# Optimization experiments

Hardware: AMD Instinct MI355X
Metric: run time of the kernel (lower is better)

The kernel has to match this reference:

```python
import jax, jax.numpy as jnp
import numpy as np

# ---- module hyperparameters (from init_kwargs / tracker defaults) ----
D_MODEL = 512
D_HEAD = 512
LAMBDA_0 = 1.0        # A_0 = I / lambda_0
FIXED_LAMBDA = 1.0    # fixed penalty magnitude -> U = sqrt(lambda) * K (then / sqrt(d_head))
STAB_EPS = 1e-6       # InversePenaltyTracker.stabilization_eps
PERIODIC_EPS = 1e-6   # InversePenaltyTracker.periodic_eps
PERIOD = 128          # InversePenaltyTracker.period (periodic re-regularization)
EXPLODE_EPS = 1e-5    # fallback_add_explode coefficient
NORM_THRESH = 1000.0  # explosion detection threshold on Frobenius norms


def setup_inputs() -> dict:
    key = jax.random.key(0)
    ks = jax.random.split(key, 9)
    B, T, d = 8, 2048, D_MODEL
    s = 1.0 / np.sqrt(d)
    f32 = jnp.float32
    return {
        "x": jax.random.normal(ks[0], (B, T, d), f32),
        "Wq": (jax.random.normal(ks[1], (D_HEAD, d), f32) * s),
        "bq": jax.random.normal(ks[2], (D_HEAD,), f32) * 0.02,
        "Wk": (jax.random.normal(ks[3], (D_HEAD, d), f32) * s),
        "bk": jax.random.normal(ks[4], (D_HEAD,), f32) * 0.02,
        "Wv": (jax.random.normal(ks[5], (D_HEAD, d), f32) * s),
        "bv": jax.random.normal(ks[6], (D_HEAD,), f32) * 0.02,
        "Wo": (jax.random.normal(ks[7], (d, D_HEAD), f32) * s),
        "bo": jax.random.normal(ks[8], (d,), f32) * 0.02,
    }


def _vla_forward(x, Wq, bq, Wk, bk, Wv, bv, Wo, bo):
    B, T, _ = x.shape
    d = D_HEAD
    # projections (nn.Linear: x @ W.T + b)
    Q = jnp.einsum('btd,hd->bth', x, Wq) + bq
    K = jnp.einsum('btd,hd->bth', x, Wk) + bk
    V = jnp.einsum('btd,hd->bth', x, Wv) + bv

    # PenaltyBuilder (rank 1, fixed lambda): u_t = sqrt(lambda) * k_t, then / sqrt(d_head)
    U = (jnp.sqrt(jnp.float32(FIXED_LAMBDA)) / jnp.sqrt(jnp.float32(d))) * K
    s_seq = jnp.sum(K * Q, axis=-1)                                   # (B,T)
    Vn = V / (jnp.linalg.norm(V, axis=-1, keepdims=True) + 1e-6)      # (B,T,d)

    I = jnp.eye(d, dtype=jnp.float32)
    A0 = jnp.zeros((B, d, d), jnp.float32) + I / LAMBDA_0
    S0 = jnp.zeros((B, d, d), jnp.float32)

    def step(carry, inp):
        A, S = carry
        q, u, s_t, vn, t = inp  # q,u,vn: (B,d); s_t: (B,); t: scalar int
        # Sherman-Morrison rank-1 inverse update with stabilization
        z = jnp.einsum('bij,bj->bi', A, u)
        dot = jnp.sum(u * z, axis=-1)
        delta = jnp.maximum(1.0 + dot, 1e-6)
        unstable = (jnp.abs(delta) < STAB_EPS) | ~jnp.isfinite(delta)
        safe = jnp.where(unstable, 1.0, delta)
        upd = (z[:, :, None] * z[:, None, :]) / safe[:, None, None]
        A = jnp.where(unstable[:, None, None], A + STAB_EPS * I, A - upd)
        # periodic re-regularization (inv_step = t+1)
        A = jnp.where(((t + 1) % PERIOD) == 0, A + PERIODIC_EPS * I, A)
        # alpha_t = s_t * (A u_t)
        z2 = jnp.einsum('bij,bj->bi', A, u)
        alpha = s_t[:, None] * z2
        # memory update S += v_norm alpha^T
        S = S + vn[:, :, None] * alpha[:, None, :]
        # explosion guard
        Sn = jnp.linalg.norm(S.reshape(S.shape[0], -1), axis=-1)
        An = jnp.linalg.norm(A.reshape(A.shape[0], -1), axis=-1)
        A = jnp.where(((Sn > NORM_THRESH) | (An > NORM_THRESH))[:, None, None],
                      A + EXPLODE_EPS * I, A)
        o = jnp.einsum('bij,bj->bi', S, q)
        return (A, S), o

    xs = (jnp.swapaxes(Q, 0, 1), jnp.swapaxes(U, 0, 1),
          jnp.swapaxes(s_seq, 0, 1), jnp.swapaxes(Vn, 0, 1),
          jnp.arange(T))
    _, O = jax.lax.scan(step, (A0, S0), xs)    # O: (T,B,d)
    O = jnp.swapaxes(O, 0, 1)                  # (B,T,d)
    return jnp.einsum('bth,dh->btd', O, Wo) + bo


def reference(x, Wq, bq, Wk, bk, Wv, bv, Wo, bo):
    return _vla_forward(x, Wq, bq, Wk, bk, Wv, bv, Wo, bo)
```

## Files before the change

### kernel.cpp

```cpp
#include <hip/hip_runtime.h>
#include <hip/hip_bf16.h>

#define BB 8
#define TT 2048
#define DD 512
#define LL 128
#define NC 16
#define ETH 512

typedef unsigned short u16;
typedef unsigned int u32;
typedef __attribute__((ext_vector_type(8))) short bf16x8v;
typedef __attribute__((ext_vector_type(4))) float f32x4v;

__device__ __forceinline__ float bf2f(u32 h) { return __uint_as_float(h << 16); }
__device__ __forceinline__ u16 f2bf(float f) {
    u32 u = __float_as_uint(f);
    u += 0x7fffu + ((u >> 16) & 1u);
    return (u16)(u >> 16);
}
__device__ __forceinline__ float wred64(float v) {
    #pragma unroll
    for (int off = 32; off; off >>= 1) v += __shfl_xor(v, off);
    return v;
// ... 253 lines not shown
            acc[i][j] = (f32x4v){0.f, 0.f, 0.f, 0.f};

    const u16* gA[4]; const u16* gB[4];
    #pragma unroll
    for (int i = 0; i < 4; ++i) {
        const int idx = i * 256 + tid, row = idx >> 3, c = idx & 7;
        const int kb = c ^ (row & 7);
        gA[i] = Ab + (size_t)row * 512 + kb * 8;
        gB[i] = Bb + (size_t)row * 512 + kb * 8;
    }
    for (int k0 = 0; k0 < 512; k0 += 64) {
        __syncthreads();
        #pragma unroll
        for (int i = 0; i < 4; ++i) {
            const int dst = (i * 256 + wave * 64) * 8;
            __builtin_amdgcn_global_load_lds(
                (__attribute__((address_space(1))) void*)(gA[i] + k0),
                (__attribute__((address_space(3))) void*)(Agh + dst), 16, 0, 0);
            __builtin_amdgcn_global_load_lds(
                (__attribute__((address_space(1))) void*)(gB[i] + k0),
                (__attribute__((address_space(3))) void*)(Bgh + dst), 16, 0, 0);
        }
        asm volatile("s_waitcnt vmcnt(0)" ::: "memory");
        __syncthreads();

        const int l15 = lane & 15, lhi = lane >> 4;
        bf16x8v af[4][2], bfr[4][2];
        #pragma unroll
        for (int mf = 0; mf < 4; ++mf) {
            const int row = wm * 64 + mf * 16 + l15, sw = (row & 7) << 4;
            #pragma unroll
            for (int ks = 0; ks < 2; ++ks) {
                const int kb2 = (ks * 64 + lhi * 16) ^ sw;
                af[mf][ks] = *(const bf16x8v*)((const char*)Agh + row * 128 + kb2);
            }
        }
        #pragma unroll
        for (int nf = 0; nf < 4; ++nf) {
            const int row = wn * 64 + nf * 16 + l15, sw = (row & 7) << 4;
            #pragma unroll
            for (int ks = 0; ks < 2; ++ks) {
                const int kb2 = (ks * 64 + lhi * 16) ^ sw;
                bfr[nf][ks] = *(const bf16x8v*)((const char*)Bgh + row * 128 + kb2);
            }
        }
        #pragma unroll
        for (int ks = 0; ks < 2; ++ks)
            #pragma unroll
            for (int mf = 0; mf < 4; ++mf)
                #pragma unroll
                for (int nf = 0; nf < 4; ++nf)
                    acc[mf][nf] = __builtin_amdgcn_mfma_f32_16x16x32_bf16(
                        af[mf][ks], bfr[nf][ks], acc[mf][nf], 0, 0, 0);
    }
    const int l15 = lane & 15, lhi = lane >> 4;
    #pragma unroll
    for (int mf = 0; mf < 4; ++mf)
        #pragma unroll
        for (int nf = 0; nf < 4; ++nf) {
            const int n = wn * 64 + nf * 16 + l15;
            #pragma unroll
            for (int r = 0; r < 4; ++r) {
                const int m = wm * 64 + mf * 16 + lhi * 4 + r;
                Cq[(size_t)m * 128 + n] = acc[mf][nf][r];
            }
        }
}

__global__ __launch_bounds__(256)
void mfk1_kernel(const u16* __restrict__ Abf, const u16* __restrict__ Ut,
                 float* __restrict__ Wm)
{
    __shared__ u16 Ah[128 * 64];
    __shared__ u16 Bh[128 * 64];
    const int tid = threadIdx.x, wave = tid >> 6, lane = tid & 63;
    const int wm = wave >> 1, wn = wave & 1;
    const int m0 = blockIdx.x * 128;
    const int bz = blockIdx.z;

    f32x4v acc[4][4];
    #pragma unroll
    for (int i = 0; i < 4; ++i)
        #pragma unroll
        for (int j = 0; j < 4; ++j)
            acc[i][j] = (f32x4v){0.f, 0.f, 0.f, 0.f};

    const u16* Abase = Abf + (size_t)bz * 262144;
    const u16* Bbase = Ut + (size_t)bz * 1048576;
    const u16* gA[4]; const u16* gB[4];
    #pragma unroll
    for (int i = 0; i < 4; ++i) {
        const int idx = i * 256 + tid, row = idx >> 3, c = idx & 7;
        const int kb = c ^ (row & 7);
        gA[i] = Abase + (size_t)(m0 + row) * 512 + kb * 8;
        gB[i] = Bbase + (size_t)row * 512 + kb * 8;
    }
    for (int k0 = 0; k0 < 512; k0 += 64) {
        __syncthreads();
        #pragma unroll
        for (int i = 0; i < 4; ++i) {
            const int dst = (i * 256 + wave * 64) * 8;
            __builtin_amdgcn_global_load_lds(
                (__attribute__((address_space(1))) void*)(gA[i] + k0),
                (__attribute__((address_space(3))) void*)(Ah + dst), 16, 0, 0);
            __builtin_amdgcn_global_load_lds(
                (__attribute__((address_space(1))) void*)(gB[i] + k0),
                (__attribute__((address_space(3))) void*)(Bh + dst), 16, 0, 0);
        }
        asm volatile("s_waitcnt vmcnt(0)" ::: "memory");
        __syncthreads();

        const int l15 = lane & 15, lhi = lane >> 4;
        bf16x8v af[4][2], bfr[4][2];
        #pragma unroll
        for (int mf = 0; mf < 4; ++mf) {
            const int row = wm * 64 + mf * 16 + l15, sw = (row & 7) << 4;
            #pragma unroll
            for (int ks = 0; ks < 2; ++ks) {
                const int kb2 = (ks * 64 + lhi * 16) ^ sw;
                af[mf][ks] = *(const bf16x8v*)((const char*)Ah + row * 128 + kb2);
            }
        }
        #pragma unroll
        for (int nf = 0; nf < 4; ++nf) {
            const int row = wn * 64 + nf * 16 + l15, sw = (row & 7) << 4;
            #pragma unroll
            for (int ks = 0; ks < 2; ++ks) {
                const int kb2 = (ks * 64 + lhi * 16) ^ sw;
                bfr[nf][ks] = *(const bf16x8v*)((const char*)Bh + row * 128 + kb2);
            }
        }
        #pragma unroll
        for (int ks = 0; ks < 2; ++ks)
            #pragma unroll
            for (int mf = 0; mf < 4; ++mf)
                #pragma unroll
                for (int nf = 0; nf < 4; ++nf)
                    acc[mf][nf] = __builtin_amdgcn_mfma_f32_16x16x32_bf16(
                        af[mf][ks], bfr[nf][ks], acc[mf][nf], 0, 0, 0);
    }
    const int l15 = lane & 15, lhi = lane >> 4;
    float* C = Wm + (size_t)bz * 65536;
    #pragma unroll
    for (int mf = 0; mf < 4; ++mf)
        #pragma unroll
        for (int nf = 0; nf < 4; ++nf) {
            const int n = wn * 64 + nf * 16 + l15;
            #pragma unroll
            for (int r = 0; r < 4; ++r) {
                const int m = m0 + wm * 64 + mf * 16 + lhi * 4 + r;
                C[(size_t)m * 128 + n] = acc[mf][nf][r];
            }
        }
}

__global__ __launch_bounds__(256)
void prep_kernel(const u16* __restrict__ Qb, const u16* __restrict__ Ub,
                 u16* __restrict__ Vb, float* __restrict__ sseq)
{
    const int lane = threadIdx.x & 63, wid = threadIdx.x >> 6;
    const int row = blockIdx.x * 4 + wid;
    const size_t base = (size_t)row * DD;
    const uint4 qr = *(const uint4*)(Qb + base + lane * 8);
    const uint4 ur = *(const uint4*)(Ub + base + lane * 8);
    const uint4 vr = *(const uint4*)(Vb + base + lane * 8);
    float q[8], u[8], v[8];
    unpack8(qr, q); unpack8(ur, u); unpack8(vr, v);
    float sd = 0.f, nv = 0.f;
    #pragma unroll
    for (int e = 0; e < 8; ++e) { sd = fmaf(q[e], u[e], sd); nv = fmaf(v[e], v[e], nv); }
    #pragma unroll
    for (int off = 32; off; off >>= 1) { sd += __shfl_xor(sd, off); nv += __shfl_xor(nv, off); }
    if (lane == 0) sseq[row] = sd * 22.627416997969522f;
    const float inv = 1.f / (sqrtf(nv) + 1e-6f);
    uint4 o;
    o.x = (u32)f2bf(v[0] * inv) | ((u32)f2bf(v[1] * inv) << 16);
    o.y = (u32)f2bf(v[2] * inv) | ((u32)f2bf(v[3] * inv) << 16);
    o.z = (u32)f2bf(v[4] * inv) | ((u32)f2bf(v[5] * inv) << 16);
    o.w = (u32)f2bf(v[6] * inv) | ((u32)f2bf(v[7] * inv) << 16);
    *(uint4*)(Vb + base + lane * 8) = o;
}

__global__ __launch_bounds__(256)
void init_kernel(float4* __restrict__ A4, float4* __restrict__ S4,
                 ushort4* __restrict__ Sbf4, ushort4* __restrict__ Abf4,
                 float* __restrict__ SnSq, float* __restrict__ AnAcc)
{
    const int gtid = blockIdx.x * 256 + threadIdx.x;
    const int N4 = BB * DD * DD / 4;
    const ushort4 z4 = {0, 0, 0, 0};
    for (int idx = gtid; idx < N4; idx += gridDim.x * 256) {
        const int e0 = idx << 2;
        const int r = (e0 >> 9) & 511;
        const int c = e0 & 511;
        float4 v;
        v.x = (c + 0 == r) ? 1.f : 0.f;
        v.y = (c + 1 == r) ? 1.f : 0.f;
        v.z = (c + 2 == r) ? 1.f : 0.f;
        v.w = (c + 3 == r) ? 1.f : 0.f;
        A4[idx] = v;
        S4[idx] = make_float4(0.f, 0.f, 0.f, 0.f);
        Sbf4[idx] = z4;
        if (Abf4) {
            ushort4 a;
            a.x = (c + 0 == r) ? 0x3F80 : 0;
            a.y = (c + 1 == r) ? 0x3F80 : 0;
            a.z = (c + 2 == r) ? 0x3F80 : 0;
            a.w = (c + 3 == r) ? 0x3F80 : 0;
            Abf4[idx] = a;
        }
    }
    if (gtid < BB) { SnSq[gtid] = 0.f; AnAcc[gtid] = 512.f; }
}

struct GP {
    int alay, blay, epi;
    const void* Ap; const void* Bp;
    void* Cp; float* Cio;
    const float* gdiag; float* anacc;
    const float* invdp; const float* cap; const float* cbp;
    const u16* Ulastp; float* Zsp; float* Alphap;
    u16* albt; u16* sbf; u16* abf;
    int lda, ldb, ldc, K;
    long sA, sB, sC, sCio;
};

__device__ __forceinline__ void gemm_body(const GP& p, const int bz) {
    __shared__ __align__(16) float As[32][68];
    __shared__ __align__(16) float Bs[32][68];
    const int m0 = blockIdx.x * 64, n0 = blockIdx.y * 64;
    const int tid = threadIdx.x, tx = tid & 15, ty = tid >> 4;
    float acc[4][4] = {};
    for (int k0 = 0; k0 < p.K; k0 += 32) {
        if (p.alay == 0) {
            const float* A = (const float*)p.Ap + (size_t)bz * p.sA;
            #pragma unroll
            for (int h = 0; h < 2; ++h) {
                const int g = tid + h * 256, m = g >> 3, k4 = (g & 7) * 4;
                const float4 r = *(const float4*)(A + (size_t)(m0 + m) * p.lda + k0 + k4);
                As[k4][m] = r.x; As[k4+1][m] = r.y; As[k4+2][m] = r.z; As[k4+3][m] = r.w;
            }
        } else if (p.alay == 2) {
            const u16* A = (const u16*)p.Ap + (size_t)bz * p.sA;
            #pragma unroll
            for (int h = 0; h < 2; ++h) {
                const int g = tid + h * 256, m = g >> 3, k4 = (g & 7) * 4;
                const ushort4 r = *(const ushort4*)(A + (size_t)(m0 + m) * p.lda + k0 + k4);
                As[k4][m]=bf2f(r.x); As[k4+1][m]=bf2f(r.y); As[k4+2][m]=bf2f(r.z); As[k4+3][m]=bf2f(r.w);
            }
        } else if (p.alay == 1 || p.alay == 4) {
            const float* A = (const float*)p.Ap + (size_t)bz * p.sA;
            #pragma unroll
            for (int h = 0; h < 2; ++h) {
                const int g = tid + h * 256, k = g >> 4, m4 = (g & 15) * 4;
                float4 r = *(const float4*)(A + (size_t)(k0 + k) * p.lda + m0 + m4);
                if (p.alay == 4) {
                    const int kg = k0 + k, mg = m0 + m4;
                    if (kg > mg + 0) r.x = 0.f;
                    if (kg > mg + 1) r.y = 0.f;
                    if (kg > mg + 2) r.z = 0.f;
                    if (kg > mg + 3) r.w = 0.f;
                }
                As[k][m4] = r.x; As[k][m4+1] = r.y; As[k][m4+2] = r.z; As[k][m4+3] = r.w;
            }
        } else {
            const u16* A = (const u16*)p.Ap + (size_t)bz * p.sA;
            #pragma unroll
            for (int h = 0; h < 2; ++h) {
                const int g = tid + h * 256, k = g >> 4, m4 = (g & 15) * 4;
                const ushort4 r = *(const ushort4*)(A + (size_t)(k0 + k) * p.lda + m0 + m4);
                As[k][m4]=bf2f(r.x); As[k][m4+1]=bf2f(r.y); As[k][m4+2]=bf2f(r.z); As[k][m4+3]=bf2f(r.w);
            }
        }
        if (p.blay == 0) {
            const float* B = (const float*)p.Bp + (size_t)bz * p.sB;
            #pragma unroll
            for (int h = 0; h < 2; ++h) {
                const int g = tid + h * 256, k = g >> 4, n4 = (g & 15) * 4;
                const float4 r = *(const float4*)(B + (size_t)(k0 + k) * p.ldb + n0 + n4);
                Bs[k][n4] = r.x; Bs[k][n4+1] = r.y; Bs[k][n4+2] = r.z; Bs[k][n4+3] = r.w;
            }
        } else if (p.blay == 2) {
            const u16* B = (const u16*)p.Bp + (size_t)bz * p.sB;
            #pragma unroll
            for (int h = 0; h < 2; ++h) {
                const int g = tid + h * 256, k = g >> 4, n4 = (g & 15) * 4;
                const ushort4 r = *(const ushort4*)(B + (size_t)(k0 + k) * p.ldb + n0 + n4);
                Bs[k][n4]=bf2f(r.x); Bs[k][n4+1]=bf2f(r.y); Bs[k][n4+2]=bf2f(r.z); Bs[k][n4+3]=bf2f(r.w);
            }
        } else if (p.blay == 1) {
            const float* B = (const float*)p.Bp + (size_t)bz * p.sB;
            #pragma unroll
            for (int h = 0; h < 2; ++h) {
                const int g = tid + h * 256, n = g >> 3, k4 = (g & 7) * 4;
                const float4 r = *(const float4*)(B + (size_t)(n0 + n) * p.ldb + k0 + k4);
                Bs[k4][n] = r.x; Bs[k4+1][n] = r.y; Bs[k4+2][n] = r.z; Bs[k4+3][n] = r.w;
            }
        } else {
            const u16* B = (const u16*)p.Bp + (size_t)bz * p.sB;
            #pragma unroll
            for (int h = 0; h < 2; ++h) {
                const int g = tid + h * 256, n = g >> 3, k4 = (g & 7) * 4;
                const ushort4 r = *(const ushort4*)(B + (size_t)(n0 + n) * p.ldb + k0 + k4);
                Bs[k4][n]=bf2f(r.x); Bs[k4+1][n]=bf2f(r.y); Bs[k4+2][n]=bf2f(r.z); Bs[k4+3][n]=bf2f(r.w);
            }
        }
        __syncthreads();
        #pragma unroll
        for (int kk = 0; kk < 32; ++kk) {
            const float4 xa = *(const float4*)&As[kk][ty * 4];
            const float4 wb = *(const float4*)&Bs[kk][tx * 4];
            const float xv[4] = {xa.x, xa.y, xa.z, xa.w};
            const float wv[4] = {wb.x, wb.y, wb.z, wb.w};
            #pragma unroll
            for (int i = 0; i < 4; ++i)
                #pragma unroll
                for (int j = 0; j < 4; ++j)
                    acc[i][j] = fmaf(xv[i], wv[j], acc[i][j]);
        }
        __syncthreads();
    }
    const int mb = m0 + ty * 4, nb = n0 + tx * 4;
    if (p.epi == 0) {
        float* C = (float*)p.Cp + (size_t)bz * p.sC;
        #pragma unroll
        for (int i = 0; i < 4; ++i)
            #pragma unroll
            for (int j = 0; j < 4; ++j)
                C[(size_t)(mb + i) * p.ldc + nb + j] = acc[i][j];
    } else if (p.epi == 1) {
        float* C = p.Cio + (size_t)bz * p.sCio;
        const float gd = p.gdiag[bz];
        float v2 = 0.f;
        #pragma unroll
        for (int i = 0; i < 4; ++i)
            #pragma unroll
            for (int j = 0; j < 4; ++j) {
                const size_t idx = (size_t)(mb + i) * p.ldc + nb + j;
                float v = C[idx] - acc[i][j] + ((mb + i) == (nb + j) ? gd : 0.f);
                C[idx] = v;
                if (p.abf) p.abf[(size_t)bz * p.sCio + idx] = f2bf(v);
                v2 = fmaf(v, v, v2);
            }
        v2 = wred64(v2);
        if ((tid & 63) == 0) atomicAdd(p.anacc + bz, v2);
    } else if (p.epi == 2) {
        float* C = p.Cio + (size_t)bz * p.sCio;
        u16* SB = p.sbf + (size_t)bz * p.sCio;
        #pragma unroll
        for (int i = 0; i < 4; ++i)
            #pragma unroll
            for (int j = 0; j < 4; ++j) {
                const size_t idx = (size_t)(mb + i) * p.ldc + nb + j;
                const float v = C[idx] + acc[i][j];
                C[idx] = v;
                SB[idx] = f2bf(v);
            }
    } else if (p.epi == 3) {
        u16* O = (u16*)p.Cp + (size_t)bz * p.sC;
        const float* OB = p.Cio + (size_t)bz * p.sCio;
        #pragma unroll
        for (int i = 0; i < 4; ++i)
            #pragma unroll
            for (int j = 0; j < 4; ++j)
                O[(size_t)(mb + i) * p.ldc + nb + j] =
                    f2bf(acc[i][j] + OB[(size_t)(nb + j) * 256 + mb + i]);
    } else {
        float* Zb  = (float*)p.Cp + (size_t)bz * 65536;
        float* Zsb = p.Zsp + (size_t)bz * 65536;
        float* Apb = p.Alphap + (size_t)bz * 65536;
        #pragma unroll
        for (int j = 0; j < 4; ++j) {
            const int n = nb + j;
            const float iv = p.invdp[bz * 128 + n];
            const float cav = p.cap[bz * 128 + n];
            const float cbv = p.cbp[bz * 128 + n];
            #pragma unroll
            for (int i = 0; i < 4; ++i) {
                const int m = mb + i;
                const float z = acc[i][j];
                const size_t o = (size_t)m * 128 + n;
                Zb[o] = z;
                Zsb[o] = z * iv;
                float a = z * cav;
                if (cbv != 0.f) a = fmaf(cbv, bf2f(p.Ulastp[(size_t)bz * 1048576 + m]), a);
                Apb[o] = a;
                p.albt[(size_t)bz * 65536 + (size_t)n * 512 + m] = f2bf(a);
            }
        }
    }
}

__global__ __launch_bounds__(256) void gemmx(GP p) { gemm_body(p, blockIdx.z); }

__global__ __launch_bounds__(256)
void lvl5_kernel(const u16* Sb, const u16* AlT, const float* Alpha,
                 const u16* Qt, const u16* Vnt,
                 float* P, float* Ga, float* Gv, float* OBSA, float* dsum)
{
    const int z = blockIdx.z;
    if (z < 8) {
        mfk6_body(Sb, Qt, AlT, Vnt, OBSA, dsum, z);
        return;
    }
    if (blockIdx.x != 0 || blockIdx.y != 0) return;
    const int zz = z - 8, b = zz / 3, j = zz - b * 3;
    const u16* Ab = (j == 2) ? (Vnt + (size_t)b * 1048576) : (AlT + (size_t)b * 65536);
    const u16* Bb = (j == 0) ? (Qt + (size_t)b * 1048576)
                  : (j == 1) ? (AlT + (size_t)b * 65536)
                             : (Vnt + (size_t)b * 1048576);
    float* Cq = ((j == 0) ? P : (j == 1) ? Ga : Gv) + (size_t)b * 16384;
    mfg_body(Ab, Bb, Cq);
}

__global__ __launch_bounds__(256)
void lvl7_kernel(const float* P, const u16* Vnt, u16* Obt, const float* OBSA,
                 const float* Alpha, const float* Zs, const float* Z,
                 float* S, u16* Sbf, float* A, u16* Abf,
                 const float* gdiag, float* AnAcc)
{
    const int z = blockIdx.z;
    GP p{};
    if (z < 8) {
        p.alay = 0; p.Ap = Zs; p.lda = 128; p.sA = 65536;
        p.blay = 1; p.Bp = Z; p.ldb = 128; p.sB = 65536;
        p.epi = 1; p.Cio = A; p.sCio = 262144; p.ldc = 512;
        p.gdiag = gdiag; p.anacc = AnAcc; p.abf = Abf; p.K = 128;
        gemm_body(p, z);
    } else if (z < 16) {
        p.alay = 3; p.Ap = Vnt; p.lda = 512; p.sA = 1048576;
        p.blay = 1; p.Bp = Alpha; p.ldb = 128; p.sB = 65536;
        p.epi = 2; p.Cio = S; p.sbf = Sbf; p.sCio = 262144; p.ldc = 512; p.K = 128;
        gemm_body(p, z - 8);
    } else {
        if (blockIdx.x >= 2) return;
        p.alay = 4; p.Ap = P; p.lda = 128; p.sA = 16384;
        p.blay = 2; p.Bp = Vnt; p.ldb = 512; p.sB = 1048576;
        p.epi = 3; p.Cp = Obt; p.ldc = 512; p.sC = 1048576;
        p.Cio = (float*)OBSA; p.sCio = 131072; p.K = 128;
        gemm_body(p, z - 16);
    }
}

__global__ __launch_bounds__(512)
void elim_kernel(const float* __restrict__ G, float* __restrict__ Tg,
                 const float* __restrict__ sseq, float* __restrict__ invd,
                 float* __restrict__ ca, float* __restrict__ cb,
                 float* __restrict__ dsum_g, const int t0)
{
    const int b = blockIdx.x, tid = threadIdx.x, lane = tid & 63, wave = tid >> 6;
    __shared__ __align__(16) float E[128][132];
    __shared__ __align__(16) float Cs[128][132];
    __shared__ __align__(16) float Scr[2368];
    __shared__ float del[128];
    float (*Tm)[132] = E;
    float (*LpT)[132] = (float(*)[132])Scr;
    float (*SpT)[132] = (float(*)[132])(Scr + 1056);

    {
        const float4* Gb = (const float4*)(G + (size_t)b * 16384);
        for (int idx = tid; idx < 4096; idx += ETH) {
            const int r = idx >> 5, c4 = idx & 31;
            ((float4*)&E[r][0])[c4] = Gb[idx];
        }
    }
    if (tid < 128) dsum_g[b * 128 + tid] = 0.f;
    __syncthreads();

    for (int p = 0; p < 16; ++p) {
        const int pc0 = p * 8;
        if (wave == 0) {
            float pr0[8], pr1[8];
            #pragma unroll
            for (int j = 0; j < 8; ++j) {
                pr0[j] = E[pc0 + j][lane];
                pr1[j] = E[pc0 + j][64 + lane];
            }
            float dl[8];
            const bool hi = (pc0 >= 64);
            #pragma unroll
            for (int j = 0; j < 8; ++j) {
                const int t = pc0 + j;
                const int pl = t & 63;
                float prow[8];
                #pragma unroll
                for (int c = 0; c < 8; ++c) {
                    const float v0 = __shfl(pr0[c], pl);
                    const float v1 = __shfl(pr1[c], pl);
                    prow[c] = hi ? v1 : v0;
                }
                const float d = fmaxf(1.f + prow[j], 1e-6f);
                dl[j] = d;
                const float inv = 1.f / d;
                if (lane > t) {
                    const float coef = pr0[j] * inv;
                    #pragma unroll
                    for (int c = j + 1; c < 8; ++c) pr0[c] = fmaf(-coef, prow[c], pr0[c]);
                }
                if (lane + 64 > t) {
                    const float coef = pr1[j] * inv;
                    #pragma unroll
                    for (int c = j + 1; c < 8; ++c) pr1[c] = fmaf(-coef, prow[c], pr1[c]);
                }
            }
            #pragma unroll
            for (int j = 0; j < 8; ++j) {
                const float idj = 1.f / dl[j];
                const int t = pc0 + j;
                {
                    const bool below = (lane > t);
                    const float y = below ? pr0[j] : 0.f;
                    const float l = y * idj;
                    LpT[j][lane] = l; SpT[j][lane] = y; Cs[t][lane] = l;
                }
                {
                    const int r = lane + 64;
                    const bool below = (r > t);
                    const float y = below ? pr1[j] : 0.f;
                    const float l = y * idj;
                    LpT[j][r] = l; SpT[j][r] = y; Cs[t][r] = l;
                }
            }
            if (lane < 8) del[pc0 + lane] = dl[lane];
        }
        __syncthreads();
        const int r0b = pc0 + 8;
        if (r0b < 128) {
            const int nrows = 128 - r0b;
            const int c40 = r0b >> 2, nc4 = 32 - c40;
            for (int idx = tid; idx < nrows * nc4; idx += ETH) {
                const int rr = idx / nc4, cc = idx - rr * nc4;
                const int r = r0b + rr, c4 = c40 + cc;
                float4 e = ((float4*)&E[r][0])[c4];
                #pragma unroll
                for (int j = 0; j < 8; ++j) {
                    const float lv = LpT[j][r];
                    const float4 sv = ((const float4*)&SpT[j][0])[c4];
                    e.x = fmaf(-lv, sv.x, e.x);
                    e.y = fmaf(-lv, sv.y, e.y);
                    e.z = fmaf(-lv, sv.z, e.z);
                    e.w = fmaf(-lv, sv.w, e.w);
                }
                ((float4*)&E[r][0])[c4] = e;
            }
        }
        __syncthreads();
    }

    for (int idx = tid; idx < 4224; idx += ETH)
        ((float4*)&Tm[0][0])[idx] = make_float4(0.f, 0.f, 0.f, 0.f);
    __syncthreads();
    if (tid < 128) Tm[tid][tid] = 1.f;
    __syncthreads();
    {
        const int g = tid >> 3, c = tid & 7;
        if (g < 16) {
            for (int r2 = c - 1; r2 >= 0; --r2) {
                float s = 0.f;
                for (int kk = r2 + 1; kk <= c; ++kk)
                    s = fmaf(Cs[8 * g + r2][8 * g + kk],
                             (kk == c) ? 1.f : Tm[8 * g + kk][8 * g + c], s);
                Tm[8 * g + r2][8 * g + c] = -s;
            }
        }
    }
    __syncthreads();
    for (int s = 8; s <= 64; s <<= 1) {
        const int npairs = 64 / s;
        const int nj = (s == 64) ? 32 : s;
        const int stride = nj + 4;
        const int nj4 = nj >> 2;
        const int Nel = npairs * s * nj4;
        const int nhalf = (s == 64) ? 2 : 1;
        for (int jh = 0; jh < nhalf; ++jh) {
            for (int idx = tid; idx < Nel; idx += ETH) {
                const int p2 = idx / (s * nj4), rem = idx - p2 * s * nj4;
                const int i = rem / nj4, j4 = rem - i * nj4;
                const int I0 = 2 * s * p2, J0 = I0 + s;
                const int jc = j4 * 4 + jh * 32;
                float4 x = make_float4(0.f, 0.f, 0.f, 0.f);
                for (int k = 0; k < s; ++k) {
                    const float cv = Cs[I0 + i][J0 + k];
                    const float4 tv = *(const float4*)&Tm[J0 + k][J0 + jc];
                    x.x = fmaf(cv, tv.x, x.x);
                    x.y = fmaf(cv, tv.y, x.y);
                    x.z = fmaf(cv, tv.z, x.z);
                    x.w = fmaf(cv, tv.w, x.w);
                }
                *(float4*)&Scr[p2 * s * stride + i * stride + j4 * 4] = x;
            }
            __syncthreads();
            for (int idx = tid; idx < Nel; idx += ETH) {
                const int p2 = idx / (s * nj4), rem = idx - p2 * s * nj4;
                const int i = rem / nj4, j4 = rem - i * nj4;
                const int I0 = 2 * s * p2, J0 = I0 + s;
                const int jc = j4 * 4 + jh * 32;
                float4 y = make_float4(0.f, 0.f, 0.f, 0.f);
                for (int k = 0; k < s; ++k) {
                    const float tv = Tm[I0 + i][I0 + k];
                    const float4 xv = *(const float4*)&Scr[p2 * s * stride + k * stride + j4 * 4];
                    y.x = fmaf(tv, xv.x, y.x);
                    y.y = fmaf(tv, xv.y, y.y);
                    y.z = fmaf(tv, xv.z, y.z);
                    y.w = fmaf(tv, xv.w, y.w);
                }
                float4 o;
                o.x = -y.x; o.y = -y.y; o.z = -y.z; o.w = -y.w;
                *(float4*)&Tm[I0 + i][J0 + jc] = o;
            }
            __syncthreads();
        }
    }
    {
        float4* Tgb = (float4*)(Tg + (size_t)b * 16384);
        for (int idx = tid; idx < 4096; idx += ETH) {
            const int r = idx >> 5, c4 = idx & 31;
            Tgb[idx] = ((const float4*)&Tm[r][0])[c4];
        }
    }
    if (tid < 128) {
        const float d = del[tid];
        const float s = sseq[(size_t)b * TT + t0 + tid];
        invd[b * 128 + tid] = 1.f / d;
        ca[b * 128 + tid] = s / d;
        cb[b * 128 + tid] = (tid == 127) ? s * 1e-6f : 0.f;
    }
}

__global__ __launch_bounds__(256)
void guard_kernel(const float* __restrict__ dsum_g, const float* __restrict__ Ga,
                  const float* __restrict__ Gv, float* __restrict__ SnSq,
                  float* __restrict__ AnAcc, float* __restrict__ gdiag)
{
    const int b = blockIdx.x, tid = threadIdx.x;
    __shared__ float rpart[256], dsh[128], mdia[128];
    const int t = tid & 127, half = tid >> 7;
    const float* gv = Gv + (size_t)b * 16384 + t * 128;
    const float* ga = Ga + (size_t)b * 16384 + t * 128;
    float rs = 0.f;
    for (int j = half; j < t; j += 2) rs = fmaf(gv[j], ga[j], rs);
    rpart[tid] = rs;
    if (half == 0) { dsh[t] = dsum_g[b * 128 + t]; mdia[t] = gv[t] * ga[t]; }
    __syncthreads();
    if (tid == 0) {
        const float An2 = AnAcc[b];
        float Sn2 = SnSq[b], D = 0.f, T = 0.f;
        int ng = 0;
        for (int t2 = 0; t2 < 128; ++t2) {
            D += dsh[t2];
            T += mdia[t2] + 2.f * (rpart[t2] + rpart[t2 + 128]);
            const float sn2 = Sn2 + 2.f * D + T;
            if (sn2 > 1e6f || An2 > 1e6f) ++ng;
        }
        SnSq[b] = Sn2 + 2.f * D + T;
        gdiag[b] = 1e-6f + (float)ng * 1e-5f;
        AnAcc[b] = 0.f;
    }
}

extern "C" void kernel_launch(void* const* d_in, const int* in_sizes, int n_in,
                              void* d_out, int out_size, void* d_ws, size_t ws_size,
                              hipStream_t stream)
{
    const float* x  = (const float*)d_in[0];
    const float* Wq = (const float*)d_in[1];
    const float* bq = (const float*)d_in[2];
    const float* Wk = (const float*)d_in[3];
    const float* bk = (const float*)d_in[4];
    const float* Wv = (const float*)d_in[5];
    const float* bv = (const float*)d_in[6];
    const float* Wo = (const float*)d_in[7];
    const float* bo = (const float*)d_in[8];

    char* ws = (char*)d_ws;
    u16* Qb    = (u16*)(ws);
    u16* Ub    = (u16*)(ws + (16ull << 20));
    u16* Vnb   = (u16*)(ws + (32ull << 20));
    u16* Ob    = (u16*)(ws + (48ull << 20));
    u16* x_bf  = Ob;
    float* A    = (float*)(ws + (64ull << 20));
    float* S    = (float*)(ws + (72ull << 20));
    float* Wm   = (float*)(ws + (80ull << 20));
    float* Z    = (float*)(ws + (82ull << 20));
    float* Zs   = (float*)(ws + (84ull << 20));
    float* Alpha= (float*)(ws + (86ull << 20));
    float* OBSA = (float*)(ws + (88ull << 20));
    float* G    = (float*)(ws + (92ull << 20));
    float* Tg   = (float*)(ws + (92ull << 20) + (512ull << 10));
    float* P    = (float*)(ws + (93ull << 20));
    float* Ga   = (float*)(ws + (93ull << 20) + (512ull << 10));
    float* Gv   = (float*)(ws + (94ull << 20));
    float* invd = (float*)(ws + (94ull << 20) + (512ull << 10));
    float* ca   = (float*)(ws + (94ull << 20) + (516ull << 10));
    float* cb   = (float*)(ws + (94ull << 20) + (520ull << 10));
    float* sseq = (float*)(ws + (94ull << 20) + (528ull << 10));
    float* SnSq = (float*)(ws + (94ull << 20) + (600ull << 10));
    float* AnAcc= (float*)(ws + (94ull << 20) + (600ull << 10) + 64);
    float* gdiag= (float*)(ws + (94ull << 20) + (600ull << 10) + 128);
    float* dsum = (float*)(ws + (94ull << 20) + (604ull << 10));
    u16* Wq_bf = (u16*)(ws + (95ull << 20));
    u16* Wk_bf = (u16*)(ws + (95ull << 20) + (512ull << 10));
    u16* Wv_bf = (u16*)(ws + (96ull << 20));
    u16* Wo_bf = (u16*)(ws + (96ull << 20) + (512ull << 10));
    u16* S_bf  = (u16*)(ws + (97ull << 20));
    u16* AlT   = (u16*)(ws + (101ull << 20));

    const bool big = (ws_size >= (111ull << 20));
    u16* A_bf = big ? (u16*)(ws + (102ull << 20)) : (u16*)nullptr;

    f2bf_kernel<<<2048, 256, 0, stream>>>((const float4*)x, (ushort4*)x_bf, 2097152);
    wconv_kernel<<<dim3(256, 4), 256, 0, stream>>>(
        (const float4*)Wq, (const float4*)Wk, (const float4*)Wv, (const float4*)Wo,
        (ushort4*)Wq_bf, (ushort4*)Wk_bf, (ushort4*)Wv_bf, (ushort4*)Wo_bf);

    mfma_gemm<1><<<dim3(128, 4), 256, 0, stream>>>(x_bf, Wq_bf, bq, Qb, 1.f);
    mfma_gemm<1><<<dim3(128, 4), 256, 0, stream>>>(x_bf, Wk_bf, bk, Ub, 0.04419417382415922f);
    mfma_gemm<1><<<dim3(128, 4), 256, 0, stream>>>(x_bf, Wv_bf, bv, Vnb, 1.f);
    prep_kernel<<<4096, 256, 0, stream>>>(Qb, Ub, Vnb, sseq);
    init_kernel<<<2048, 256, 0, stream>>>((float4*)A, (float4*)S, (ushort4*)S_bf,
                                          (ushort4*)A_bf, SnSq, AnAcc);

    for (int c = 0; c < NC; ++c) {
        const int t0 = c * LL;
        const u16* Ut = Ub + (size_t)t0 * 512;
        const u16* Qt = Qb + (size_t)t0 * 512;
        const u16* Vt = Vnb + (size_t)t0 * 512;
        if (big) {
            mfk1_kernel<<<dim3(4, 1, 8), 256, 0, stream>>>(A_bf, Ut, Wm);
        } else {
            GP p1{}; p1.alay = 0; p1.Ap = A; p1.lda = 512; p1.sA = 262144;
            p1.blay = 3; p1.Bp = Ut; p1.ldb = 512; p1.sB = 1048576;
            p1.epi = 0; p1.Cp = Wm; p1.ldc = 128; p1.sC = 65536; p1.K = 512;
            gemmx<<<dim3(8, 2, 8), 256, 0, stream>>>(p1);
        }
        GP p2{}; p2.alay = 2; p2.Ap = Ut; p2.lda = 512; p2.sA = 1048576;
        p2.blay = 0; p2.Bp = Wm; p2.ldb = 128; p2.sB = 65536;
        p2.epi = 0; p2.Cp = G; p2.ldc = 128; p2.sC = 16384; p2.K = 512;
        gemmx<<<dim3(2, 2, 8), 256, 0, stream>>>(p2);
        elim_kernel<<<8, 512, 0, stream>>>(G, Tg, sseq, invd, ca, cb, dsum, t0);
        GP p4{}; p4.alay = 0; p4.Ap = Wm; p4.lda = 128; p4.sA = 65536;
        p4.blay = 0; p4.Bp = Tg; p4.ldb = 128; p4.sB = 16384;
        p4.epi = 4; p4.Cp = Z; p4.Zsp = Zs; p4.Alphap = Alpha; p4.albt = AlT;
        p4.invdp = invd; p4.cap = ca; p4.cbp = cb;
        p4.Ulastp = Ub + (size_t)(t0 + 127) * 512;
        p4.K = 128; p4.ldc = 128; p4.sC = 65536;
        gemmx<<<dim3(8, 2, 8), 256, 0, stream>>>(p4);
        lvl5_kernel<<<dim3(4, 2, 32), 256, 0, stream>>>(S_bf, AlT, Alpha, Qt, Vt,
            P, Ga, Gv, OBSA, dsum);
        guard_kernel<<<8, 256, 0, stream>>>(dsum, Ga, Gv, SnSq, AnAcc, gdiag);
        lvl7_kernel<<<dim3(8, 8, 24), 256, 0, stream>>>(P, Vt, Ob + (size_t)t0 * 512, OBSA,
            Alpha, Zs, Z, S, S_bf, A, A_bf, gdiag, AnAcc);
    }
    mfma_gemm<0><<<dim3(128, 4), 256, 0, stream>>>(Ob, Wo_bf, bo, d_out, 1.f);
}
```

Measured before the change: 3.105 ms.

## Move A and S rank-128 updates to MFMA with split-bf16 precision

Replaces the fp32 SIMT GEMMs that apply the chunked rank-128 updates to A and S with bf16 MFMA kernels using LDS direct loads. The A update keeps near-fp32 accuracy by splitting Z and Zs into hi/lo bf16 parts and summing three MFMA products. The epilogue now writes the bf16 split operands, and a Vn transpose is folded into a merged guard/output kernel so the MFMA operands are K-contiguous. This trades extra bf16 buffers, a transpose, and a small precision loss on the S update for much cheaper matrix math on the per-chunk critical path.

```diff
diff --git a/kernel.cpp b/kernel.cpp
--- a/kernel.cpp
+++ b/kernel.cpp
@@ -429,6 +429,226 @@
                 C[(size_t)m * 128 + n] = acc[mf][nf][r];
             }
         }
+}
+
+__device__ __forceinline__ void mfk10_body(char* smemc,
+    const u16* __restrict__ Zshi, const u16* __restrict__ Zslo,
+    const u16* __restrict__ Zhi, const u16* __restrict__ Zlo,
+    float* __restrict__ A, u16* __restrict__ Abf,
+    const float* __restrict__ gdiag, float* __restrict__ AnAcc, const int bz)
+{
+    u16* Ah = (u16*)smemc;
+    u16* Al = (u16*)(smemc + 16384);
+    u16* Bh = (u16*)(smemc + 32768);
+    u16* Bl = (u16*)(smemc + 49152);
+    const int tid = threadIdx.x, wave = tid >> 6, lane = tid & 63;
+    const int wm = wave >> 1, wn = wave & 1;
+    const int m0 = blockIdx.x * 128, n0 = blockIdx.y * 128;
+
+    f32x4v acc[4][4];
+    #pragma unroll
+    for (int i = 0; i < 4; ++i)
+        #pragma unroll
+        for (int j = 0; j < 4; ++j)
+            acc[i][j] = (f32x4v){0.f, 0.f, 0.f, 0.f};
+
+    const u16* Ahb = Zshi + (size_t)bz * 65536;
+    const u16* Alb = Zslo + (size_t)bz * 65536;
+    const u16* Bhb = Zhi + (size_t)bz * 65536;
+    const u16* Blb = Zlo + (size_t)bz * 65536;
+    const u16* gAh[4]; const u16* gAl[4]; const u16* gBh[4]; const u16* gBl[4];
+    #pragma unroll
+    for (int i = 0; i < 4; ++i) {
+        const int idx = i * 256 + tid, row = idx >> 3, c = idx & 7;
+        const int kb = c ^ (row & 7);
+        gAh[i] = Ahb + (size_t)(m0 + row) * 128 + kb * 8;
+        gAl[i] = Alb + (size_t)(m0 + row) * 128 + kb * 8;
+        gBh[i] = Bhb + (size_t)(n0 + row) * 128 + kb * 8;
+        gBl[i] = Blb + (size_t)(n0 + row) * 128 + kb * 8;
+    }
+    for (int k0 = 0; k0 < 128; k0 += 64) {
+        __syncthreads();
+        #pragma unroll
+        for (int i = 0; i < 4; ++i) {
+            const int dst = (i * 256 + wave * 64) * 8;
+            __builtin_amdgcn_global_load_lds(
+                (__attribute__((address_space(1))) void*)(gAh[i] + k0),
+                (__attribute__((address_space(3))) void*)(Ah + dst), 16, 0, 0);
+            __builtin_amdgcn_global_load_lds(
+                (__attribute__((address_space(1))) void*)(gAl[i] + k0),
+                (__attribute__((address_space(3))) void*)(Al + dst), 16, 0, 0);
+            __builtin_amdgcn_global_load_lds(
+                (__attribute__((address_space(1))) void*)(gBh[i] + k0),
+                (__attribute__((address_space(3))) void*)(Bh + dst), 16, 0, 0);
+            __builtin_amdgcn_global_load_lds(
+                (__attribute__((address_space(1))) void*)(gBl[i] + k0),
+                (__attribute__((address_space(3))) void*)(Bl + dst), 16, 0, 0);
+        }
+        asm volatile("s_waitcnt vmcnt(0)" ::: "memory");
+        __syncthreads();
+
+        const int l15 = lane & 15, lhi = lane >> 4;
+        bf16x8v ah[4][2], al[4][2], bh[4][2], bl[4][2];
+        #pragma unroll
+        for (int mf = 0; mf < 4; ++mf) {
+            const int row = wm * 64 + mf * 16 + l15, sw = (row & 7) << 4;
+            #pragma unroll
+            for (int ks = 0; ks < 2; ++ks) {
+                const int kb2 = (ks * 64 + lhi * 16) ^ sw;
+                ah[mf][ks] = *(const bf16x8v*)((const char*)Ah + row * 128 + kb2);
+                al[mf][ks] = *(const bf16x8v*)((const char*)Al + row * 128 + kb2);
+            }
+        }
+        #pragma unroll
+        for (int nf = 0; nf < 4; ++nf) {
+            const int row = wn * 64 + nf * 16 + l15, sw = (row & 7) << 4;
+            #pragma unroll
+            for (int ks = 0; ks < 2; ++ks) {
+                const int kb2 = (ks * 64 + lhi * 16) ^ sw;
+                bh[nf][ks] = *(const bf16x8v*)((const char*)Bh + row * 128 + kb2);
+                bl[nf][ks] = *(const bf16x8v*)((const char*)Bl + row * 128 + kb2);
+            }
+        }
+        #pragma unroll
+        for (int ks = 0; ks < 2; ++ks)
+            #pragma unroll
+            for (int mf = 0; mf < 4; ++mf)
+                #pragma unroll
+                for (int nf = 0; nf < 4; ++nf) {
+                    acc[mf][nf] = __builtin_amdgcn_mfma_f32_16x16x32_bf16(
+                        ah[mf][ks], bh[nf][ks], acc[mf][nf], 0, 0, 0);
+                    acc[mf][nf] = __builtin_amdgcn_mfma_f32_16x16x32_bf16(
+                        al[mf][ks], bh[nf][ks], acc[mf][nf], 0, 0, 0);
+                    acc[mf][nf] = __builtin_amdgcn_mfma_f32_16x16x32_bf16(
+                        ah[mf][ks], bl[nf][ks], acc[mf][nf], 0, 0, 0);
+                }
+    }
+    const int l15 = lane & 15, lhi = lane >> 4;
+    float* Ab = A + (size_t)bz * 262144;
+    u16* Abfb = Abf ? (Abf + (size_t)bz * 262144) : (u16*)nullptr;
+    const float gd = gdiag[bz];
+    float v2 = 0.f;
+    #pragma unroll
+    for (int mf = 0; mf < 4; ++mf)
+        #pragma unroll
+        for (int nf = 0; nf < 4; ++nf) {
+            const int n = n0 + wn * 64 + nf * 16 + l15;
+            #pragma unroll
+            for (int r = 0; r < 4; ++r) {
+                const int m = m0 + wm * 64 + mf * 16 + lhi * 4 + r;
+                const size_t idx = (size_t)m * 512 + n;
+                const float v = Ab[idx] - acc[mf][nf][r] + ((m == n) ? gd : 0.f);
+                Ab[idx] = v;
+                if (Abfb) Abfb[idx] = f2bf(v);
+                v2 = fmaf(v, v, v2);
+            }
+        }
+    v2 = wred64(v2);
+    if (lane == 0) atomicAdd(AnAcc + bz, v2);
+}
+
+__device__ __forceinline__ void mfk9_body(char* smemc,
+    const u16* __restrict__ VnTc, const u16* __restrict__ Alphab,
+    float* __restrict__ S, u16* __restrict__ Sbf, const int bz)
+{
+    u16* Ah = (u16*)smemc;
+    u16* Bh = (u16*)(smemc + 16384);
+    const int tid = threadIdx.x, wave = tid >> 6, lane = tid & 63;
+    const int wm = wave >> 1, wn = wave & 1;
+    const int m0 = blockIdx.x * 128, n0 = blockIdx.y * 128;
+
+    f32x4v acc[4][4];
+    #pragma unroll
+    for (int i = 0; i < 4; ++i)
+        #pragma unroll
+        for (int j = 0; j < 4; ++j)
+            acc[i][j] = (f32x4v){0.f, 0.f, 0.f, 0.f};
+
+    const u16* Ab = VnTc + (size_t)bz * 65536;
+    const u16* Bb = Alphab + (size_t)bz * 65536;
+    const u16* gA[4]; const u16* gB[4];
+    #pragma unroll
+    for (int i = 0; i < 4; ++i) {
+        const int idx = i * 256 + tid, row = idx >> 3, c = idx & 7;
+        const int kb = c ^ (row & 7);
+        gA[i] = Ab + (size_t)(m0 + row) * 128 + kb * 8;
+        gB[i] = Bb + (size_t)(n0 + row) * 128 + kb * 8;
+    }
+    for (int k0 = 0; k0 < 128; k0 += 64) {
+        __syncthreads();
+        #pragma unroll
+        for (int i = 0; i < 4; ++i) {
+            const int dst = (i * 256 + wave * 64) * 8;
+            __builtin_amdgcn_global_load_lds(
+                (__attribute__((address_space(1))) void*)(gA[i] + k0),
+                (__attribute__((address_space(3))) void*)(Ah + dst), 16, 0, 0);
+            __builtin_amdgcn_global_load_lds(
+                (__attribute__((address_space(1))) void*)(gB[i] + k0),
+                (__attribute__((address_space(3))) void*)(Bh + dst), 16, 0, 0);
+        }
+        asm volatile("s_waitcnt vmcnt(0)" ::: "memory");
+        __syncthreads();
+
+        const int l15 = lane & 15, lhi = lane >> 4;
+        bf16x8v af[4][2], bfr[4][2];
+        #pragma unroll
+        for (int mf = 0; mf < 4; ++mf) {
+            const int row = wm * 64 + mf * 16 + l15, sw = (row & 7) << 4;
+            #pragma unroll
+            for (int ks = 0; ks < 2; ++ks) {
+                const int kb2 = (ks * 64 + lhi * 16) ^ sw;
+                af[mf][ks] = *(const bf16x8v*)((const char*)Ah + row * 128 + kb2);
+            }
+        }
+        #pragma unroll
+        for (int nf = 0; nf < 4; ++nf) {
+            const int row = wn * 64 + nf * 16 + l15, sw = (row & 7) << 4;
+            #pragma unroll
+            for (int ks = 0; ks < 2; ++ks) {
+                const int kb2 = (ks * 64 + lhi * 16) ^ sw;
+                bfr[nf][ks] = *(const bf16x8v*)((const char*)Bh + row * 128 + kb2);
+            }
+        }
+        #pragma unroll
+        for (int ks = 0; ks < 2; ++ks)
+            #pragma unroll
+            for (int mf = 0; mf < 4; ++mf)
+                #pragma unroll
+                for (int nf = 0; nf < 4; ++nf)
+                    acc[mf][nf] = __builtin_amdgcn_mfma_f32_16x16x32_bf16(
+                        af[mf][ks], bfr[nf][ks], acc[mf][nf], 0, 0, 0);
+    }
+    const int l15 = lane & 15, lhi = lane >> 4;
+    float* Sb = S + (size_t)bz * 262144;
+    u16* Sbfb = Sbf + (size_t)bz * 262144;
+    #pragma unroll
+    for (int mf = 0; mf < 4; ++mf)
+        #pragma unroll
+        for (int nf = 0; nf < 4; ++nf) {
+            const int n = n0 + wn * 64 + nf * 16 + l15;
+            #pragma unroll
+            for (int r = 0; r < 4; ++r) {
+                const int m = m0 + wm * 64 + mf * 16 + lhi * 4 + r;
+                const size_t idx = (size_t)m * 512 + n;
+                const float v = Sb[idx] + acc[mf][nf][r];
+                Sb[idx] = v;
+                Sbfb[idx] = f2bf(v);
+            }
+        }
+}
+
+__global__ __launch_bounds__(256)
+void lvl7a_kernel(const u16* Zshi, const u16* Zslo, const u16* Zhi, const u16* Zlo,
+                  float* A, u16* Abf, const float* gdiag, float* AnAcc,
+                  const u16* VnTc, const u16* Alphab, float* S, u16* Sbf)
+{
+    __shared__ __align__(16) char smem[65536];
+    const int z = blockIdx.z;
+    if (z < 8) {
+        mfk10_body(smem, Zshi, Zslo, Zhi, Zlo, A, Abf, gdiag, AnAcc, z);
+    } else {
+        mfk9_body(smem, VnTc, Alphab, S, Sbf, z - 8);
+    }
 }
 
 __global__ __launch_bounds__(256)
@@ -496,8 +716,8 @@
     void* Cp; float* Cio;
     const float* gdiag; float* anacc;
     const float* invdp; const float* cap; const float* cbp;
-    const u16* Ulastp; float* Zsp; float* Alphap;
-    u16* albt; u16* sbf; u16* abf;
+    const u16* Ulastp;
+    u16 *zhi, *zlo, *zshi, *zslo, *alb, *albt;
     int lda, ldb, ldc, K;
     long sA, sB, sC, sCio;
 };
@@ -605,34 +825,6 @@
             #pragma unroll
             for (int j = 0; j < 4; ++j)
                 C[(size_t)(mb + i) * p.ldc + nb + j] = acc[i][j];
-    } else if (p.epi == 1) {
-        float* C = p.Cio + (size_t)bz * p.sCio;
-        const float gd = p.gdiag[bz];
-        float v2 = 0.f;
-        #pragma unroll
-        for (int i = 0; i < 4; ++i)
-            #pragma unroll
-            for (int j = 0; j < 4; ++j) {
-                const size_t idx = (size_t)(mb + i) * p.ldc + nb + j;
-                float v = C[idx] - acc[i][j] + ((mb + i) == (nb + j) ? gd : 0.f);
-                C[idx] = v;
-                if (p.abf) p.abf[(size_t)bz * p.sCio + idx] = f2bf(v);
-                v2 = fmaf(v, v, v2);
-            }
-        v2 = wred64(v2);
-        if ((tid & 63) == 0) atomicAdd(p.anacc + bz, v2);
-    } else if (p.epi == 2) {
-        float* C = p.Cio + (size_t)bz * p.sCio;
-        u16* SB = p.sbf + (size_t)bz * p.sCio;
-        #pragma unroll
-        for (int i = 0; i < 4; ++i)
-            #pragma unroll
-            for (int j = 0; j < 4; ++j) {
-                const size_t idx = (size_t)(mb + i) * p.ldc + nb + j;
-                const float v = C[idx] + acc[i][j];
-                C[idx] = v;
-                SB[idx] = f2bf(v);
-            }
     } else if (p.epi == 3) {
         u16* O = (u16*)p.Cp + (size_t)bz * p.sC;
         const float* OB = p.Cio + (size_t)bz * p.sCio;
@@ -643,9 +835,7 @@
                 O[(size_t)(mb + i) * p.ldc + nb + j] =
                     f2bf(acc[i][j] + OB[(size_t)(nb + j) * 256 + mb + i]);
     } else {
-        float* Zb  = (float*)p.Cp + (size_t)bz * 65536;
-        float* Zsb = p.Zsp + (size_t)bz * 65536;
-        float* Apb = p.Alphap + (size_t)bz * 65536;
+        const size_t o0 = (size_t)bz * 65536;
         #pragma unroll
         for (int j = 0; j < 4; ++j) {
             const int n = nb + j;
@@ -656,13 +846,16 @@
             for (int i = 0; i < 4; ++i) {
                 const int m = mb + i;
                 const float z = acc[i][j];
-                const size_t o = (size_t)m * 128 + n;
-                Zb[o] = z;
-                Zsb[o] = z * iv;
+                const float zs = z * iv;
                 float a = z * cav;
                 if (cbv != 0.f) a = fmaf(cbv, bf2f(p.Ulastp[(size_t)bz * 1048576 + m]), a);
-                Apb[o] = a;
-                p.albt[(size_t)bz * 65536 + (size_t)n * 512 + m] = f2bf(a);
+                const size_t o = o0 + (size_t)m * 128 + n;
+                const u16 zh = f2bf(z);
+                p.zhi[o] = zh; p.zlo[o] = f2bf(z - bf2f(zh));
+                const u16 sh = f2bf(zs);
+                p.zshi[o] = sh; p.zslo[o] = f2bf(zs - bf2f(sh));
+                p.alb[o] = f2bf(a);
+                p.albt[o0 + (size_t)n * 512 + m] = f2bf(a);
             }
         }
     }
@@ -671,7 +864,7 @@
 __global__ __launch_bounds__(256) void gemmx(GP p) { gemm_body(p, blockIdx.z); }
 
 __global__ __launch_bounds__(256)
-void lvl5_kernel(const u16* Sb, const u16* AlT, const float* Alpha,
+void lvl5_kernel(const u16* Sb, const u16* AlT,
                  const u16* Qt, const u16* Vnt,
                  float* P, float* Ga, float* Gv, float* OBSA, float* dsum)
 {
@@ -691,31 +884,72 @@
 }
 
 __global__ __launch_bounds__(256)
-void lvl7_kernel(const float* P, const u16* Vnt, u16* Obt, const float* OBSA,
-                 const float* Alpha, const float* Zs, const float* Z,
-                 float* S, u16* Sbf, float* A, u16* Abf,
-                 const float* gdiag, float* AnAcc)
-{
-    const int z = blockIdx.z;
-    GP p{};
+void guard_tr_kernel(const float* __restrict__ dsum_g, const float* __restrict__ Ga,
+                     const float* __restrict__ Gv, float* __restrict__ SnSq,
+                     float* __restrict__ AnAcc, float* __restrict__ gdiag,
+                     const float* __restrict__ P, const u16* __restrict__ Vnt,
+                     u16* __restrict__ Obt, const float* __restrict__ OBSA,
+                     u16* __restrict__ VnTc)
+{
+    const int z = blockIdx.z, tid = threadIdx.x;
     if (z < 8) {
-        p.alay = 0; p.Ap = Zs; p.lda = 128; p.sA = 65536;
-        p.blay = 1; p.Bp = Z; p.ldb = 128; p.sB = 65536;
-        p.epi = 1; p.Cio = A; p.sCio = 262144; p.ldc = 512;
-        p.gdiag = gdiag; p.anacc = AnAcc; p.abf = Abf; p.K = 128;
-        gemm_body(p, z);
-    } else if (z < 16) {
-        p.alay = 3; p.Ap = Vnt; p.lda = 512; p.sA = 1048576;
-        p.blay = 1; p.Bp = Alpha; p.ldb = 128; p.sB = 65536;
-        p.epi = 2; p.Cio = S; p.sbf = Sbf; p.sCio = 262144; p.ldc = 512; p.K = 128;
-        gemm_body(p, z - 8);
-    } else {
-        if (blockIdx.x >= 2) return;
+        GP p{};
         p.alay = 4; p.Ap = P; p.lda = 128; p.sA = 16384;
         p.blay = 2; p.Bp = Vnt; p.ldb = 512; p.sB = 1048576;
         p.epi = 3; p.Cp = Obt; p.ldc = 512; p.sC = 1048576;
         p.Cio = (float*)OBSA; p.sCio = 131072; p.K = 128;
-        gemm_body(p, z - 16);
+        gemm_body(p, z);
+        return;
+    }
+    if (z < 16) {
+        if (blockIdx.x != 0 || blockIdx.y != 0) return;
+        const int b = z - 8;
+        __shared__ float rpart[256], dsh[128], mdia[128];
+        const int t = tid & 127, half = tid >> 7;
+        const float* gv = Gv + (size_t)b * 16384 + t * 128;
+        const float* ga = Ga + (size_t)b * 16384 + t * 128;
+        float rs = 0.f;
+        for (int j = half; j < t; j += 2) rs = fmaf(gv[j], ga[j], rs);
+        rpart[tid] = rs;
+        if (half == 0) { dsh[t] = dsum_g[b * 128 + t]; mdia[t] = gv[t] * ga[t]; }
+        __syncthreads();
+        if (tid == 0) {
+            const float An2 = AnAcc[b];
+            float Sn2 = SnSq[b], D = 0.f, T = 0.f;
+            int ng = 0;
+            for (int t2 = 0; t2 < 128; ++t2) {
+                D += dsh[t2];
+                T += mdia[t2] + 2.f * (rpart[t2] + rpart[t2 + 128]);
+                const float sn2 = Sn2 + 2.f * D + T;
+                if (sn2 > 1e6f || An2 > 1e6f) ++ng;
+            }
+            SnSq[b] = Sn2 + 2.f * D + T;
+            gdiag[b] = 1e-6f + (float)ng * 1e-5f;
+            AnAcc[b] = 0.f;
+        }
+        return;
+    }
+    if (blockIdx.x != 0 || blockIdx.y >= 4) return;
+    const int b = z - 16, d0 = blockIdx.y * 128;
+    __shared__ u16 tile[64][65];
+    const u16* Vn = Vnt + (size_t)b * 1048576;
+    u16* VT = VnTc + (size_t)b * 65536;
+    const int c = tid & 63, rbase = tid >> 6;
+    for (int sd = 0; sd < 2; ++sd) {
+        for (int st = 0; st < 2; ++st) {
+            #pragma unroll
+            for (int rr = 0; rr < 16; ++rr) {
+                const int r = rbase + rr * 4;
+                tile[r][c] = Vn[(size_t)(st * 64 + r) * 512 + d0 + sd * 64 + c];
+            }
+            __syncthreads();
+            #pragma unroll
+            for (int rr = 0; rr < 16; ++rr) {
+                const int r2 = rbase + rr * 4;
+                VT[(size_t)(d0 + sd * 64 + r2) * 128 + st * 64 + c] = tile[c][r2];
+            }
+            __syncthreads();
+        }
     }
 }
 
@@ -904,37 +1138,6 @@
     }
 }
 
-__global__ __launch_bounds__(256)
-void guard_kernel(const float* __restrict__ dsum_g, const float* __restrict__ Ga,
-                  const float* __restrict__ Gv, float* __restrict__ SnSq,
-                  float* __restrict__ AnAcc, float* __restrict__ gdiag)
-{
-    const int b = blockIdx.x, tid = threadIdx.x;
-    __shared__ float rpart[256], dsh[128], mdia[128];
-    const int t = tid & 127, half = tid >> 7;
-    const float* gv = Gv + (size_t)b * 16384 + t * 128;
-    const float* ga = Ga + (size_t)b * 16384 + t * 128;
-    float rs = 0.f;
-    for (int j = half; j < t; j += 2) rs = fmaf(gv[j], ga[j], rs);
-    rpart[tid] = rs;
-    if (half == 0) { dsh[t] = dsum_g[b * 128 + t]; mdia[t] = gv[t] * ga[t]; }
-    __syncthreads();
-    if (tid == 0) {
-        const float An2 = AnAcc[b];
-        float Sn2 = SnSq[b], D = 0.f, T = 0.f;
-        int ng = 0;
-        for (int t2 = 0; t2 < 128; ++t2) {
-            D += dsh[t2];
-            T += mdia[t2] + 2.f * (rpart[t2] + rpart[t2 + 128]);
-            const float sn2 = Sn2 + 2.f * D + T;
-            if (sn2 > 1e6f || An2 > 1e6f) ++ng;
-        }
-        SnSq[b] = Sn2 + 2.f * D + T;
-        gdiag[b] = 1e-6f + (float)ng * 1e-5f;
-        AnAcc[b] = 0.f;
-    }
-}
-
 extern "C" void kernel_launch(void* const* d_in, const int* in_sizes, int n_in,
                               void* d_out, int out_size, void* d_ws, size_t ws_size,
                               hipStream_t stream)
@@ -958,9 +1161,12 @@
     float* A    = (float*)(ws + (64ull << 20));
     float* S    = (float*)(ws + (72ull << 20));
     float* Wm   = (float*)(ws + (80ull << 20));
-    float* Z    = (float*)(ws + (82ull << 20));
-    float* Zs   = (float*)(ws + (84ull << 20));
-    float* Alpha= (float*)(ws + (86ull << 20));
+    u16* Zhi   = (u16*)(ws + (82ull << 20));
+    u16* Zlo   = (u16*)(ws + (83ull << 20));
+    u16* Zshi  = (u16*)(ws + (84ull << 20));
+    u16* Zslo  = (u16*)(ws + (85ull << 20));
+    u16* Alphab= (u16*)(ws + (86ull << 20));
+    u16* VnTc  = (u16*)(ws + (87ull << 20));
     float* OBSA = (float*)(ws + (88ull << 20));
     float* G    = (float*)(ws + (92ull << 20));
     float* Tg   = (float*)(ws + (92ull << 20) + (512ull << 10));
@@ -1017,16 +1223,19 @@
         elim_kernel<<<8, 512, 0, stream>>>(G, Tg, sseq, invd, ca, cb, dsum, t0);
         GP p4{}; p4.alay = 0; p4.Ap = Wm; p4.lda = 128; p4.sA = 65536;
         p4.blay = 0; p4.Bp = Tg; p4.ldb = 128; p4.sB = 16384;
-        p4.epi = 4; p4.Cp = Z; p4.Zsp = Zs; p4.Alphap = Alpha; p4.albt = AlT;
+        p4.epi = 4;
+        p4.zhi = Zhi; p4.zlo = Zlo; p4.zshi = Zshi; p4.zslo = Zslo;
+        p4.alb = Alphab; p4.albt = AlT;
         p4.invdp = invd; p4.cap = ca; p4.cbp = cb;
         p4.Ulastp = Ub + (size_t)(t0 + 127) * 512;
-        p4.K = 128; p4.ldc = 128; p4.sC = 65536;
+        p4.K = 128; p4.ldc = 128;
         gemmx<<<dim3(8, 2, 8), 256, 0, stream>>>(p4);
-        lvl5_kernel<<<dim3(4, 2, 32), 256, 0, stream>>>(S_bf, AlT, Alpha, Qt, Vt,
+        lvl5_kernel<<<dim3(4, 2, 32), 256, 0, stream>>>(S_bf, AlT, Qt, Vt,
             P, Ga, Gv, OBSA, dsum);
-        guard_kernel<<<8, 256, 0, stream>>>(dsum, Ga, Gv, SnSq, AnAcc, gdiag);
-        lvl7_kernel<<<dim3(8, 8, 24), 256, 0, stream>>>(P, Vt, Ob + (size_t)t0 * 512, OBSA,
-            Alpha, Zs, Z, S, S_bf, A, A_bf, gdiag, AnAcc);
+        guard_tr_kernel<<<dim3(2, 8, 24), 256, 0, stream>>>(dsum, Ga, Gv, SnSq, AnAcc,
+            gdiag, P, Vt, Ob + (size_t)t0 * 512, OBSA, VnTc);
+        lvl7a_kernel<<<dim3(4, 4, 16), 256, 0, stream>>>(Zshi, Zslo, Zhi, Zlo,
+            A, A_bf, gdiag, AnAcc, VnTc, Alphab, S, S_bf);
     }
     mfma_gemm<0><<<dim3(128, 4), 256, 0, stream>>>(Ob, Wo_bf, bo, d_out, 1.f);
 }
```

Result: faster. 2.967 ms (-4.5%).
